# Performance work log

Measured on AMD Instinct MI355X. Metric: run time of the kernel, lower is better.

Reference implementation:

```python
import jax, jax.numpy as jnp
import numpy as np

B, T, C = 4, 2048, 384
NUM_HEADS, HEAD_SIZE = 6, 64


def setup_inputs() -> dict:
    key = jax.random.key(0)
    ks = jax.random.split(key, 6)
    s = 1.0 / np.sqrt(C)
    return {
        "x": jax.random.normal(ks[0], (B, T, C), dtype=jnp.float32),
        "Wq": jax.random.normal(ks[1], (C, NUM_HEADS * HEAD_SIZE), dtype=jnp.float32) * s,
        "bq": jnp.zeros((NUM_HEADS * HEAD_SIZE,), dtype=jnp.float32),
        "Wk": jax.random.normal(ks[2], (C, NUM_HEADS * HEAD_SIZE), dtype=jnp.float32) * s,
        "bk": jnp.zeros((NUM_HEADS * HEAD_SIZE,), dtype=jnp.float32),
        "Wv": jax.random.normal(ks[3], (C, NUM_HEADS * HEAD_SIZE), dtype=jnp.float32) * s,
        "bv": jnp.zeros((NUM_HEADS * HEAD_SIZE,), dtype=jnp.float32),
        "Wo": jax.random.normal(ks[4], (NUM_HEADS * HEAD_SIZE, C), dtype=jnp.float32) * s,
        "bo": jnp.zeros((C,), dtype=jnp.float32),
    }


def reference(x, Wq, bq, Wk, bk, Wv, bv, Wo, bo):
    b, t, c = x.shape
    h, d = NUM_HEADS, HEAD_SIZE
    q = (x @ Wq + bq).reshape(b, t, h, d)
    k = (x @ Wk + bk).reshape(b, t, h, d)
    v = (x @ Wv + bv).reshape(b, t, h, d)
    scores = jnp.einsum('bthd,bshd->bhts', q, k) / jnp.sqrt(jnp.float32(d))
    causal = jnp.tril(jnp.ones((t, t), dtype=bool))  # [t,t]
    scores = jnp.where(causal, scores, -jnp.inf)
    weights = jax.nn.softmax(scores, axis=-1)  # dropout identity (inference)
    ctx = jnp.einsum('bhts,bshd->bthd', weights, v).reshape(b, t, h * d)
    return ctx @ Wo + bo
```

## Files before the change

kernel.cpp:

```cpp
#include <hip/hip_runtime.h>

#define B_  4
#define T_  2048
#define C_  384
#define NH_ 6
#define HS_ 64
#define M_  (B_*T_)

typedef float floatx4 __attribute__((ext_vector_type(4)));
typedef __bf16 bf16x8 __attribute__((ext_vector_type(8)));
typedef unsigned short ushort_t;
typedef unsigned short ushortx8 __attribute__((ext_vector_type(8)));
typedef unsigned short ushortx4 __attribute__((ext_vector_type(4)));

__device__ __forceinline__ ushort_t f2bf(float f) {
    unsigned u = __builtin_bit_cast(unsigned, f);
    unsigned r = (u + 0x7FFFu + ((u >> 16) & 1u)) >> 16;
    return (ushort_t)r;
}

__global__ __launch_bounds__(256) void prep(
    const float* __restrict__ Wq, const float* __restrict__ Wk,
    const float* __restrict__ Wv, const float* __restrict__ Wo,
    ushort_t* __restrict__ Wtq, ushort_t* __restrict__ Wtk,
    ushort_t* __restrict__ Wtv, ushort_t* __restrict__ Wto)
{
    __shared__ float Ls[64][65];
    const int tid = threadIdx.x;
    const int idx = blockIdx.x;
    const int z = idx / 36, rest = idx % 36;
    const float* __restrict__ W = (z == 0) ? Wq : (z == 1) ? Wk : (z == 2) ? Wv : Wo;
    ushort_t* __restrict__ Wt   = (z == 0) ? Wtq : (z == 1) ? Wtk : (z == 2) ? Wtv : Wto;
    const int k0 = (rest / 6) * 64, n0 = (rest % 6) * 64;

    #pragma unroll
    for (int p = 0; p < 4; ++p) {
        const int kk = p * 16 + (tid >> 4);
        const int nn = (tid & 15) * 4;
        const float4 v = *(const float4*)&W[(size_t)(k0 + kk) * 384 + n0 + nn];
        Ls[kk][nn] = v.x; Ls[kk][nn + 1] = v.y; Ls[kk][nn + 2] = v.z; Ls[kk][nn + 3] = v.w;
    }
    __syncthreads();
    #pragma unroll
    for (int p = 0; p < 4; ++p) {
        const int n = p * 16 + (tid >> 4);
        const int kc = (tid & 15) * 4;
        ushortx4 pk;
        #pragma unroll
        for (int t = 0; t < 4; ++t) pk[t] = f2bf(Ls[kc + t][n]);
        *(ushortx4*)&Wt[(size_t)(n0 + n) * 384 + k0 + kc] = pk;
    }
}

__global__ __launch_bounds__(256) void qkv_gemm(
    const float* __restrict__ x,
    const ushort_t* __restrict__ Wtq, const ushort_t* __restrict__ Wtk,
    const ushort_t* __restrict__ Wtv,
    const float* __restrict__ bq, const float* __restrict__ bk, const float* __restrict__ bv,
    ushort_t* __restrict__ Qb, ushort_t* __restrict__ Kb, ushort_t* __restrict__ Vtb)
{
    __shared__ ushort_t Sm[2 * 128 * 32];

    const int tid  = threadIdx.x;
    const int lane = tid & 63;
    const int wv   = tid >> 6;
    const int m    = lane & 15;
    const int quad = lane >> 4;

    const int t0 = blockIdx.x * 128;
    const int n0 = blockIdx.y * 128;
    const int which = n0 / 384;
    const int n_in0 = n0 % 384;
    const bool isV = (which == 2);

    const ushort_t* __restrict__ Wt = (which == 0) ? Wtq : (which == 1) ? Wtk : Wtv;

    const int aOff = isV ? 0 : 4096;
    const int bOff = isV ? 4096 : 0;
    const int a0 = (wv & 1) * 64;
    const int b0 = (wv >> 1) * 64;

    floatx4 acc[4][4];
    #pragma unroll
    for (int i = 0; i < 4; ++i)
        #pragma unroll
        for (int j = 0; j < 4; ++j) acc[i][j] = (floatx4){0.f, 0.f, 0.f, 0.f};

    for (int k0 = 0; k0 < 384; k0 += 32) {
        __syncthreads();
        #pragma unroll
        for (int u = 0; u < 2; ++u) {
            const int e = tid + u * 256;
            const int r = e >> 2, c = e & 3;
            const int sw = ((c ^ ((r >> 1) & 3)) << 3);
            const float4 xa = *(const float4*)&x[(size_t)(t0 + r) * 384 + k0 + c * 8];
            const float4 xc = *(const float4*)&x[(size_t)(t0 + r) * 384 + k0 + c * 8 + 4];
            ushortx8 xp;
            xp[0] = f2bf(xa.x); xp[1] = f2bf(xa.y); xp[2] = f2bf(xa.z); xp[3] = f2bf(xa.w);
            xp[4] = f2bf(xc.x); xp[5] = f2bf(xc.y); xp[6] = f2bf(xc.z); xp[7] = f2bf(xc.w);
            *(ushortx8*)&Sm[r * 32 + sw] = xp;
            *(ushortx8*)&Sm[4096 + r * 32 + sw] =
                *(const ushortx8*)&Wt[(size_t)(n_in0 + r) * 384 + k0 + c * 8];
        }
        __syncthreads();

        bf16x8 fA[4], fB[4];
        #pragma unroll
        for (int i = 0; i < 4; ++i) {
            const int ra = a0 + i * 16 + m;
            fA[i] = *(const bf16x8*)&Sm[aOff + ra * 32 + ((quad ^ ((ra >> 1) & 3)) << 3)];
        }
        #pragma unroll
        for (int j = 0; j < 4; ++j) {
            const int rb = b0 + j * 16 + m;
            fB[j] = *(const bf16x8*)&Sm[bOff + rb * 32 + ((quad ^ ((rb >> 1) & 3)) << 3)];
        }
        #pragma unroll
        for (int i = 0; i < 4; ++i)
            #pragma unroll
            for (int j = 0; j < 4; ++j)
                acc[i][j] = __builtin_amdgcn_mfma_f32_16x16x32_bf16(fA[i], fB[j], acc[i][j], 0, 0, 0);
    }

    if (!isV) {
        ushort_t* __restrict__ out = (which == 0) ? Qb : Kb;
        const float* __restrict__ bias = (which == 0) ? bq : bk;
        const float scale = (which == 0) ? 0.125f : 1.0f;
        #pragma unroll
        for (int i = 0; i < 4; ++i) {
            const int n_base = n_in0 + a0 + i * 16 + quad * 4;
            const int h = n_base >> 6, d0 = n_base & 63;
            #pragma unroll
            for (int j = 0; j < 4; ++j) {
                const int tg = t0 + b0 + j * 16 + m;
                const int b = tg >> 11, tb = tg & (T_ - 1);
                ushortx4 pk;
                #pragma unroll
                for (int r = 0; r < 4; ++r)
                    pk[r] = f2bf((acc[i][j][r] + bias[n_base + r]) * scale);
                *(ushortx4*)&out[(((size_t)(b * NH_ + h)) * T_ + tb) * HS_ + d0] = pk;
            }
        }
    } else {
        #pragma unroll
        for (int i = 0; i < 4; ++i) {
            const int tg0 = t0 + a0 + i * 16 + quad * 4;
            const int b = tg0 >> 11, tb0 = tg0 & (T_ - 1);
            #pragma unroll
            for (int j = 0; j < 4; ++j) {
                const int n_l = n_in0 + b0 + j * 16 + m;
                const int h = n_l >> 6, d = n_l & 63;
                const float bb = bv[n_l];
                ushortx4 pk;
                #pragma unroll
                for (int r = 0; r < 4; ++r) pk[r] = f2bf(acc[i][j][r] + bb);
                *(ushortx4*)&Vtb[(((size_t)(b * NH_ + h)) * HS_ + d) * T_ + tb0] = pk;
            }
        }
    }
}

__global__ __launch_bounds__(256) void proj_gemm(
    const ushort_t* __restrict__ ctxb,
    const ushort_t* __restrict__ Wto,
    const float* __restrict__ bo,
    float* __restrict__ out)
{
    __shared__ ushort_t Sm[2 * 128 * 32];

    const int tid  = threadIdx.x;
    const int lane = tid & 63;
    const int wv   = tid >> 6;
    const int m    = lane & 15;
    const int quad = lane >> 4;

    const int t0 = blockIdx.x * 128;
    const int n0 = blockIdx.y * 128;
    const int a0 = (wv & 1) * 64;
    const int b0 = (wv >> 1) * 64;

    floatx4 acc[4][4];
    #pragma unroll
    for (int i = 0; i < 4; ++i)
        #pragma unroll
        for (int j = 0; j < 4; ++j) acc[i][j] = (floatx4){0.f, 0.f, 0.f, 0.f};

    for (int k0 = 0; k0 < 384; k0 += 32) {
        __syncthreads();
        #pragma unroll
        for (int u = 0; u < 2; ++u) {
            const int e = tid + u * 256;
            const int r = e >> 2, c = e & 3;
            const int sw = ((c ^ ((r >> 1) & 3)) << 3);
            *(ushortx8*)&Sm[r * 32 + sw] =
                *(const ushortx8*)&ctxb[(size_t)(t0 + r) * 384 + k0 + c * 8];
            *(ushortx8*)&Sm[4096 + r * 32 + sw] =
                *(const ushortx8*)&Wto[(size_t)(n0 + r) * 384 + k0 + c * 8];
        }
        __syncthreads();

        bf16x8 fA[4], fB[4];
        #pragma unroll
        for (int i = 0; i < 4; ++i) {
            const int ra = a0 + i * 16 + m;
            fA[i] = *(const bf16x8*)&Sm[4096 + ra * 32 + ((quad ^ ((ra >> 1) & 3)) << 3)];
        }
        #pragma unroll
        for (int j = 0; j < 4; ++j) {
            const int rb = b0 + j * 16 + m;
            fB[j] = *(const bf16x8*)&Sm[rb * 32 + ((quad ^ ((rb >> 1) & 3)) << 3)];
        }
        #pragma unroll
        for (int i = 0; i < 4; ++i)
            #pragma unroll
            for (int j = 0; j < 4; ++j)
                acc[i][j] = __builtin_amdgcn_mfma_f32_16x16x32_bf16(fA[i], fB[j], acc[i][j], 0, 0, 0);
    }

    #pragma unroll
    for (int i = 0; i < 4; ++i) {
        const int n_base = n0 + a0 + i * 16 + quad * 4;
        const float4 bb = *(const float4*)&bo[n_base];
        #pragma unroll
        for (int j = 0; j < 4; ++j) {
            const int tg = t0 + b0 + j * 16 + m;
            float4 o;
            o.x = acc[i][j][0] + bb.x;
            o.y = acc[i][j][1] + bb.y;
            o.z = acc[i][j][2] + bb.z;
            o.w = acc[i][j][3] + bb.w;
            *(float4*)&out[(size_t)tg * 384 + n_base] = o;
        }
    }
}

__global__ __launch_bounds__(256) void attn_mfma(
    const ushort_t* __restrict__ Q,
    const ushort_t* __restrict__ K,
    const ushort_t* __restrict__ Vt,
    ushort_t* __restrict__ ctx)
{
    __shared__ ushort_t Ks[2][64 * 64];
    __shared__ ushort_t Vs[2][64 * 64];
    __shared__ ushort_t Ps[4][16 * 64];

    const int tid  = threadIdx.x;
    const int lane = tid & 63;
    const int wv   = tid >> 6;
    const int m    = lane & 15;
    const int quad = lane >> 4;
    const int cA   = (quad ^ (m & 7)) << 3;

    const int p = blockIdx.x;
    const int h = blockIdx.y, b = blockIdx.z;
    const int bh = b * NH_ + h;

    const int tileHi = 63 - p;
    const int rowbase = ((wv < 2) ? tileHi : p) * 32 + (wv & 1) * 16;
    const int myext = rowbase >> 6;
    const int blockext = tileHi >> 1;

    const ushort_t* __restrict__ Kg = K  + (size_t)bh * (T_ * HS_);
    const ushort_t* __restrict__ Vg = Vt + (size_t)bh * (HS_ * T_);

    const int r0 = tid >> 3,        c0 = tid & 7;
    const int r1 = (tid + 256) >> 3, c1 = tid & 7;
    const int sw0 = ((c0 ^ (r0 & 7)) << 3);
    const int sw1 = ((c1 ^ (r1 & 7)) << 3);

    bf16x8 qf0, qf1;
    {
        const ushort_t* qp = Q + ((size_t)bh * T_ + rowbase + m) * HS_;
        qf0 = *(const bf16x8*)(qp + quad * 8);
        qf1 = *(const bf16x8*)(qp + 32 + quad * 8);
    }

    floatx4 acc_o[4];
    #pragma unroll
    for (int dt = 0; dt < 4; ++dt) acc_o[dt] = (floatx4){0.f, 0.f, 0.f, 0.f};
    float l_lane[4] = {0.f, 0.f, 0.f, 0.f};

    ushort_t* __restrict__ Pw = &Ps[wv][0];

    ushortx8 kr0 = *(const ushortx8*)&Kg[(size_t)r0 * HS_ + c0 * 8];
    ushortx8 kr1 = *(const ushortx8*)&Kg[(size_t)r1 * HS_ + c1 * 8];
    ushortx8 vr0 = *(const ushortx8*)&Vg[(size_t)r0 * T_ + c0 * 8];
    ushortx8 vr1 = *(const ushortx8*)&Vg[(size_t)r1 * T_ + c1 * 8];

    for (int kt = 0; kt <= blockext; ++kt) {
        ushort_t* __restrict__ Kc = &Ks[kt & 1][0];
        ushort_t* __restrict__ Vc = &Vs[kt & 1][0];
        *(ushortx8*)&Kc[r0 * 64 + sw0] = kr0;
        *(ushortx8*)&Kc[r1 * 64 + sw1] = kr1;
        *(ushortx8*)&Vc[r0 * 64 + sw0] = vr0;
        *(ushortx8*)&Vc[r1 * 64 + sw1] = vr1;

        if (kt < blockext) {
            const int s1 = (kt + 1) * 64;
            kr0 = *(const ushortx8*)&Kg[(size_t)(s1 + r0) * HS_ + c0 * 8];
            kr1 = *(const ushortx8*)&Kg[(size_t)(s1 + r1) * HS_ + c1 * 8];
            vr0 = *(const ushortx8*)&Vg[(size_t)r0 * T_ + s1 + c0 * 8];
            vr1 = *(const ushortx8*)&Vg[(size_t)r1 * T_ + s1 + c1 * 8];
        }
        __syncthreads();

        if (kt > myext) continue;

        floatx4 s[4];
        #pragma unroll
        for (int kc = 0; kc < 4; ++kc) {
            const int kb = (kc * 16 + m) * 64;
            bf16x8 k0 = *(const bf16x8*)&Kc[kb + cA];
            bf16x8 k1 = *(const bf16x8*)&Kc[kb + (cA ^ 32)];
            floatx4 a = (floatx4){0.f, 0.f, 0.f, 0.f};
            a = __builtin_amdgcn_mfma_f32_16x16x32_bf16(qf0, k0, a, 0, 0, 0);
            a = __builtin_amdgcn_mfma_f32_16x16x32_bf16(qf1, k1, a, 0, 0, 0);
            s[kc] = a;
        }

        if (kt == myext) {
            #pragma unroll
            for (int kc = 0; kc < 4; ++kc) {
                const int key = kt * 64 + kc * 16 + m;
                #pragma unroll
                for (int r = 0; r < 4; ++r)
                    if (key > rowbase + quad * 4 + r) s[kc][r] = -1e30f;
            }
        }

        const int mc = m >> 3, mp = m & 7;
        #pragma unroll
        for (int r = 0; r < 4; ++r) {
            const int prow = quad * 4 + r;
            const int psw = prow & 7;
            const float p0 = __expf(s[0][r]);
            const float p1 = __expf(s[1][r]);
            const float p2 = __expf(s[2][r]);
            const float p3 = __expf(s[3][r]);
            l_lane[r] += (p0 + p1) + (p2 + p3);
            const int pb = prow * 64 + mp;
            Pw[pb + (((0 + mc) ^ psw) << 3)] = f2bf(p0);
            Pw[pb + (((2 + mc) ^ psw) << 3)] = f2bf(p1);
            Pw[pb + (((4 + mc) ^ psw) << 3)] = f2bf(p2);
            Pw[pb + (((6 + mc) ^ psw) << 3)] = f2bf(p3);
        }
        asm volatile("s_waitcnt lgkmcnt(0)" ::: "memory");
        bf16x8 pf0 = *(const bf16x8*)&Pw[m * 64 + cA];
        bf16x8 pf1 = *(const bf16x8*)&Pw[m * 64 + (cA ^ 32)];

        #pragma unroll
        for (int dt = 0; dt < 4; ++dt) {
            const int vb = (dt * 16 + m) * 64;
            bf16x8 v0 = *(const bf16x8*)&Vc[vb + cA];
            bf16x8 v1 = *(const bf16x8*)&Vc[vb + (cA ^ 32)];
            acc_o[dt] = __builtin_amdgcn_mfma_f32_16x16x32_bf16(pf0, v0, acc_o[dt], 0, 0, 0);
            acc_o[dt] = __builtin_amdgcn_mfma_f32_16x16x32_bf16(pf1, v1, acc_o[dt], 0, 0, 0);
        }
    }

    float l[4];
    #pragma unroll
    for (int r = 0; r < 4; ++r) {
        float ls = l_lane[r];
        ls += __shfl_xor(ls, 1, 64);
        ls += __shfl_xor(ls, 2, 64);
        ls += __shfl_xor(ls, 4, 64);
        ls += __shfl_xor(ls, 8, 64);
        l[r] = ls;
    }
    #pragma unroll
    for (int dt = 0; dt < 4; ++dt) {
        #pragma unroll
        for (int r = 0; r < 4; ++r) {
            const int t = rowbase + quad * 4 + r;
            ctx[((size_t)(b * T_) + t) * C_ + h * HS_ + dt * 16 + m] =
                f2bf(acc_o[dt][r] / l[r]);
        }
    }
}

extern "C" void kernel_launch(void* const* d_in, const int* in_sizes, int n_in,
                              void* d_out, int out_size, void* d_ws, size_t ws_size,
                              hipStream_t stream) {
    const float* x  = (const float*)d_in[0];
    const float* Wq = (const float*)d_in[1];
    const float* bq = (const float*)d_in[2];
    const float* Wk = (const float*)d_in[3];
    const float* bk = (const float*)d_in[4];
    const float* Wv = (const float*)d_in[5];
    const float* bv = (const float*)d_in[6];
    const float* Wo = (const float*)d_in[7];
    const float* bo = (const float*)d_in[8];
    float* out = (float*)d_out;

    const size_t per = (size_t)B_ * NH_ * T_ * HS_;
    const size_t wsz = 384 * 384;
    ushort_t* Wtq = (ushort_t*)d_ws;
    ushort_t* Wtk = Wtq + wsz;
    ushort_t* Wtv = Wtk + wsz;
    ushort_t* Wto = Wtv + wsz;
    ushort_t* Qb  = Wto + wsz;
    ushort_t* Kb  = Qb + per;
    ushort_t* Vtb = Kb + per;
    ushort_t* ctxb = Vtb + per;

    prep<<<dim3(144), 256, 0, stream>>>(Wq, Wk, Wv, Wo, Wtq, Wtk, Wtv, Wto);

    qkv_gemm<<<dim3(M_ / 128, 1152 / 128), 256, 0, stream>>>(
        x, Wtq, Wtk, Wtv, bq, bk, bv, Qb, Kb, Vtb);

    attn_mfma<<<dim3(32, NH_, B_), 256, 0, stream>>>(Qb, Kb, Vtb, ctxb);

    proj_gemm<<<dim3(M_ / 128, 384 / 128), 256, 0, stream>>>(ctxb, Wto, bo, out);
}
```

Baseline: 157.8 us.

## Pre-convert x to bf16, double-buffer GEMM smem, shrink proj tile

Adds an x-to-bf16 conversion pass to the prep kernel so qkv_gemm loads bf16 directly rather than converting fp32 in every N-tile block. Both GEMMs switch to double-buffered shared memory with register prefetch of the next K-slice, which removes one barrier per iteration. proj_gemm uses 64-row tiles to double its grid for better occupancy. In the attention kernel the barrier moves ahead of the global prefetch. The change adds a workspace buffer and an extra full pass over x.

```diff
diff --git a/kernel.cpp b/kernel.cpp
--- a/kernel.cpp
+++ b/kernel.cpp
@@ -20,6 +20,7 @@
 }
 
 __global__ __launch_bounds__(256) void prep(
+    const float* __restrict__ x, ushort_t* __restrict__ xb,
     const float* __restrict__ Wq, const float* __restrict__ Wk,
     const float* __restrict__ Wv, const float* __restrict__ Wo,
     ushort_t* __restrict__ Wtq, ushort_t* __restrict__ Wtk,
@@ -27,7 +28,20 @@
 {
     __shared__ float Ls[64][65];
     const int tid = threadIdx.x;
-    const int idx = blockIdx.x;
+    const int bx = blockIdx.x;
+
+    if (bx < 1536) {
+        const int i = (bx * 256 + tid) * 8;
+        const float4 a = *(const float4*)&x[i];
+        const float4 b = *(const float4*)&x[i + 4];
+        ushortx8 p;
+        p[0] = f2bf(a.x); p[1] = f2bf(a.y); p[2] = f2bf(a.z); p[3] = f2bf(a.w);
+        p[4] = f2bf(b.x); p[5] = f2bf(b.y); p[6] = f2bf(b.z); p[7] = f2bf(b.w);
+        *(ushortx8*)&xb[i] = p;
+        return;
+    }
+
+    const int idx = bx - 1536;
     const int z = idx / 36, rest = idx % 36;
     const float* __restrict__ W = (z == 0) ? Wq : (z == 1) ? Wk : (z == 2) ? Wv : Wo;
     ushort_t* __restrict__ Wt   = (z == 0) ? Wtq : (z == 1) ? Wtk : (z == 2) ? Wtv : Wto;
@@ -53,13 +67,13 @@
 }
 
 __global__ __launch_bounds__(256) void qkv_gemm(
-    const float* __restrict__ x,
+    const ushort_t* __restrict__ xb,
     const ushort_t* __restrict__ Wtq, const ushort_t* __restrict__ Wtk,
     const ushort_t* __restrict__ Wtv,
     const float* __restrict__ bq, const float* __restrict__ bk, const float* __restrict__ bv,
     ushort_t* __restrict__ Qb, ushort_t* __restrict__ Kb, ushort_t* __restrict__ Vtb)
 {
-    __shared__ ushort_t Sm[2 * 128 * 32];
+    __shared__ ushort_t Sm[2][8192];
 
     const int tid  = threadIdx.x;
     const int lane = tid & 63;
@@ -80,40 +94,48 @@
     const int a0 = (wv & 1) * 64;
     const int b0 = (wv >> 1) * 64;
 
+    const int rs0 = tid >> 2,         cs0 = tid & 3;
+    const int rs1 = (tid + 256) >> 2, cs1 = tid & 3;
+    const int sw0 = ((cs0 ^ ((rs0 >> 1) & 3)) << 3);
+    const int sw1 = ((cs1 ^ ((rs1 >> 1) & 3)) << 3);
+
     floatx4 acc[4][4];
     #pragma unroll
     for (int i = 0; i < 4; ++i)
         #pragma unroll
         for (int j = 0; j < 4; ++j) acc[i][j] = (floatx4){0.f, 0.f, 0.f, 0.f};
 
-    for (int k0 = 0; k0 < 384; k0 += 32) {
+    ushortx8 xr0 = *(const ushortx8*)&xb[(size_t)(t0 + rs0) * 384 + cs0 * 8];
+    ushortx8 xr1 = *(const ushortx8*)&xb[(size_t)(t0 + rs1) * 384 + cs1 * 8];
+    ushortx8 wr0 = *(const ushortx8*)&Wt[(size_t)(n_in0 + rs0) * 384 + cs0 * 8];
+    ushortx8 wr1 = *(const ushortx8*)&Wt[(size_t)(n_in0 + rs1) * 384 + cs1 * 8];
+
+    for (int ks = 0; ks < 12; ++ks) {
+        ushort_t* __restrict__ S = &Sm[ks & 1][0];
+        *(ushortx8*)&S[rs0 * 32 + sw0] = xr0;
+        *(ushortx8*)&S[rs1 * 32 + sw1] = xr1;
+        *(ushortx8*)&S[4096 + rs0 * 32 + sw0] = wr0;
+        *(ushortx8*)&S[4096 + rs1 * 32 + sw1] = wr1;
         __syncthreads();
-        #pragma unroll
-        for (int u = 0; u < 2; ++u) {
-            const int e = tid + u * 256;
-            const int r = e >> 2, c = e & 3;
-            const int sw = ((c ^ ((r >> 1) & 3)) << 3);
-            const float4 xa = *(const float4*)&x[(size_t)(t0 + r) * 384 + k0 + c * 8];
-            const float4 xc = *(const float4*)&x[(size_t)(t0 + r) * 384 + k0 + c * 8 + 4];
-            ushortx8 xp;
-            xp[0] = f2bf(xa.x); xp[1] = f2bf(xa.y); xp[2] = f2bf(xa.z); xp[3] = f2bf(xa.w);
-            xp[4] = f2bf(xc.x); xp[5] = f2bf(xc.y); xp[6] = f2bf(xc.z); xp[7] = f2bf(xc.w);
-            *(ushortx8*)&Sm[r * 32 + sw] = xp;
-            *(ushortx8*)&Sm[4096 + r * 32 + sw] =
-                *(const ushortx8*)&Wt[(size_t)(n_in0 + r) * 384 + k0 + c * 8];
-        }
-        __syncthreads();
+
+        if (ks < 11) {
+            const int kk = (ks + 1) * 32;
+            xr0 = *(const ushortx8*)&xb[(size_t)(t0 + rs0) * 384 + kk + cs0 * 8];
+            xr1 = *(const ushortx8*)&xb[(size_t)(t0 + rs1) * 384 + kk + cs1 * 8];
+            wr0 = *(const ushortx8*)&Wt[(size_t)(n_in0 + rs0) * 384 + kk + cs0 * 8];
+            wr1 = *(const ushortx8*)&Wt[(size_t)(n_in0 + rs1) * 384 + kk + cs1 * 8];
+        }
 
         bf16x8 fA[4], fB[4];
         #pragma unroll
         for (int i = 0; i < 4; ++i) {
             const int ra = a0 + i * 16 + m;
-            fA[i] = *(const bf16x8*)&Sm[aOff + ra * 32 + ((quad ^ ((ra >> 1) & 3)) << 3)];
+            fA[i] = *(const bf16x8*)&S[aOff + ra * 32 + ((quad ^ ((ra >> 1) & 3)) << 3)];
         }
         #pragma unroll
         for (int j = 0; j < 4; ++j) {
             const int rb = b0 + j * 16 + m;
-            fB[j] = *(const bf16x8*)&Sm[bOff + rb * 32 + ((quad ^ ((rb >> 1) & 3)) << 3)];
+            fB[j] = *(const bf16x8*)&S[bOff + rb * 32 + ((quad ^ ((rb >> 1) & 3)) << 3)];
         }
         #pragma unroll
         for (int i = 0; i < 4; ++i)
@@ -166,7 +188,7 @@
     const float* __restrict__ bo,
     float* __restrict__ out)
 {
-    __shared__ ushort_t Sm[2 * 128 * 32];
+    __shared__ ushort_t Sm[2][6144];
 
     const int tid  = threadIdx.x;
     const int lane = tid & 63;
@@ -174,46 +196,57 @@
     const int m    = lane & 15;
     const int quad = lane >> 4;
 
-    const int t0 = blockIdx.x * 128;
+    const int t0 = blockIdx.x * 64;
     const int n0 = blockIdx.y * 128;
     const int a0 = (wv & 1) * 64;
-    const int b0 = (wv >> 1) * 64;
-
-    floatx4 acc[4][4];
+    const int b0 = (wv >> 1) * 32;
+
+    const int rc = tid >> 2,          cc = tid & 3;
+    const int rw0 = tid >> 2,         cw0 = tid & 3;
+    const int rw1 = (tid + 256) >> 2, cw1 = tid & 3;
+    const int swc  = ((cc  ^ ((rc  >> 1) & 3)) << 3);
+    const int sww0 = ((cw0 ^ ((rw0 >> 1) & 3)) << 3);
+    const int sww1 = ((cw1 ^ ((rw1 >> 1) & 3)) << 3);
+
+    floatx4 acc[4][2];
     #pragma unroll
     for (int i = 0; i < 4; ++i)
         #pragma unroll
-        for (int j = 0; j < 4; ++j) acc[i][j] = (floatx4){0.f, 0.f, 0.f, 0.f};
-
-    for (int k0 = 0; k0 < 384; k0 += 32) {
+        for (int j = 0; j < 2; ++j) acc[i][j] = (floatx4){0.f, 0.f, 0.f, 0.f};
+
+    ushortx8 cr  = *(const ushortx8*)&ctxb[(size_t)(t0 + rc) * 384 + cc * 8];
+    ushortx8 wr0 = *(const ushortx8*)&Wto[(size_t)(n0 + rw0) * 384 + cw0 * 8];
+    ushortx8 wr1 = *(const ushortx8*)&Wto[(size_t)(n0 + rw1) * 384 + cw1 * 8];
+
+    for (int ks = 0; ks < 12; ++ks) {
+        ushort_t* __restrict__ S = &Sm[ks & 1][0];
+        *(ushortx8*)&S[rc * 32 + swc] = cr;
+        *(ushortx8*)&S[2048 + rw0 * 32 + sww0] = wr0;
+        *(ushortx8*)&S[2048 + rw1 * 32 + sww1] = wr1;
         __syncthreads();
-        #pragma unroll
-        for (int u = 0; u < 2; ++u) {
-            const int e = tid + u * 256;
-            const int r = e >> 2, c = e & 3;
-            const int sw = ((c ^ ((r >> 1) & 3)) << 3);
-            *(ushortx8*)&Sm[r * 32 + sw] =
-                *(const ushortx8*)&ctxb[(size_t)(t0 + r) * 384 + k0 + c * 8];
-            *(ushortx8*)&Sm[4096 + r * 32 + sw] =
-                *(const ushortx8*)&Wto[(size_t)(n0 + r) * 384 + k0 + c * 8];
-        }
-        __syncthreads();
-
-        bf16x8 fA[4], fB[4];
+
+        if (ks < 11) {
+            const int kk = (ks + 1) * 32;
+            cr  = *(const ushortx8*)&ctxb[(size_t)(t0 + rc) * 384 + kk + cc * 8];
+            wr0 = *(const ushortx8*)&Wto[(size_t)(n0 + rw0) * 384 + kk + cw0 * 8];
+            wr1 = *(const ushortx8*)&Wto[(size_t)(n0 + rw1) * 384 + kk + cw1 * 8];
+        }
+
+        bf16x8 fA[4], fB[2];
         #pragma unroll
         for (int i = 0; i < 4; ++i) {
             const int ra = a0 + i * 16 + m;
-            fA[i] = *(const bf16x8*)&Sm[4096 + ra * 32 + ((quad ^ ((ra >> 1) & 3)) << 3)];
-        }
-        #pragma unroll
-        for (int j = 0; j < 4; ++j) {
+            fA[i] = *(const bf16x8*)&S[2048 + ra * 32 + ((quad ^ ((ra >> 1) & 3)) << 3)];
+        }
+        #pragma unroll
+        for (int j = 0; j < 2; ++j) {
             const int rb = b0 + j * 16 + m;
-            fB[j] = *(const bf16x8*)&Sm[rb * 32 + ((quad ^ ((rb >> 1) & 3)) << 3)];
+            fB[j] = *(const bf16x8*)&S[rb * 32 + ((quad ^ ((rb >> 1) & 3)) << 3)];
         }
         #pragma unroll
         for (int i = 0; i < 4; ++i)
             #pragma unroll
-            for (int j = 0; j < 4; ++j)
+            for (int j = 0; j < 2; ++j)
                 acc[i][j] = __builtin_amdgcn_mfma_f32_16x16x32_bf16(fA[i], fB[j], acc[i][j], 0, 0, 0);
     }
 
@@ -222,7 +255,7 @@
         const int n_base = n0 + a0 + i * 16 + quad * 4;
         const float4 bb = *(const float4*)&bo[n_base];
         #pragma unroll
-        for (int j = 0; j < 4; ++j) {
+        for (int j = 0; j < 2; ++j) {
             const int tg = t0 + b0 + j * 16 + m;
             float4 o;
             o.x = acc[i][j][0] + bb.x;
@@ -263,7 +296,7 @@
     const ushort_t* __restrict__ Kg = K  + (size_t)bh * (T_ * HS_);
     const ushort_t* __restrict__ Vg = Vt + (size_t)bh * (HS_ * T_);
 
-    const int r0 = tid >> 3,        c0 = tid & 7;
+    const int r0 = tid >> 3,         c0 = tid & 7;
     const int r1 = (tid + 256) >> 3, c1 = tid & 7;
     const int sw0 = ((c0 ^ (r0 & 7)) << 3);
     const int sw1 = ((c1 ^ (r1 & 7)) << 3);
@@ -294,6 +327,7 @@
         *(ushortx8*)&Kc[r1 * 64 + sw1] = kr1;
         *(ushortx8*)&Vc[r0 * 64 + sw0] = vr0;
         *(ushortx8*)&Vc[r1 * 64 + sw1] = vr1;
+        __syncthreads();
 
         if (kt < blockext) {
             const int s1 = (kt + 1) * 64;
@@ -302,7 +336,6 @@
             vr0 = *(const ushortx8*)&Vg[(size_t)r0 * T_ + s1 + c0 * 8];
             vr1 = *(const ushortx8*)&Vg[(size_t)r1 * T_ + s1 + c1 * 8];
         }
-        __syncthreads();
 
         if (kt > myext) continue;
 
@@ -395,7 +428,8 @@
 
     const size_t per = (size_t)B_ * NH_ * T_ * HS_;
     const size_t wsz = 384 * 384;
-    ushort_t* Wtq = (ushort_t*)d_ws;
+    ushort_t* xb  = (ushort_t*)d_ws;
+    ushort_t* Wtq = xb + per;
     ushort_t* Wtk = Wtq + wsz;
     ushort_t* Wtv = Wtk + wsz;
     ushort_t* Wto = Wtv + wsz;
@@ -404,12 +438,13 @@
     ushort_t* Vtb = Kb + per;
     ushort_t* ctxb = Vtb + per;
 
-    prep<<<dim3(144), 256, 0, stream>>>(Wq, Wk, Wv, Wo, Wtq, Wtk, Wtv, Wto);
+    prep<<<dim3(1536 + 144), 256, 0, stream>>>(
+        x, xb, Wq, Wk, Wv, Wo, Wtq, Wtk, Wtv, Wto);
 
     qkv_gemm<<<dim3(M_ / 128, 1152 / 128), 256, 0, stream>>>(
-        x, Wtq, Wtk, Wtv, bq, bk, bv, Qb, Kb, Vtb);
+        xb, Wtq, Wtk, Wtv, bq, bk, bv, Qb, Kb, Vtb);
 
     attn_mfma<<<dim3(32, NH_, B_), 256, 0, stream>>>(Qb, Kb, Vtb, ctxb);
 
-    proj_gemm<<<dim3(M_ / 128, 384 / 128), 256, 0, stream>>>(ctxb, Wto, bo, out);
-}
+    proj_gemm<<<dim3(M_ / 64, 384 / 128), 256, 0, stream>>>(ctxb, Wto, bo, out);
+}
```

Measured after the change: 150.5 us. 1.05x faster.
